# Kernel tuning notes

Hardware: AMD Instinct MI355X
Metric: run time of the kernel (lower is better)

Reference implementation:

```python
import jax, jax.numpy as jnp
import numpy as np
from jax import lax

B, T, DIN, E, F, U, H1, DOUT = 128, 1000, 64, 256, 64, 2, 80, 64
CLIP = 5.0
LVMIN = float(np.log(1e-4))


def _gru(wih, whh, bih, bhh, x, h):
    # PyTorch GRUCell math: gates ordered [r, z, n]
    gi = x @ wih.T + bih
    gh = h @ whh.T + bhh
    ir, iz, inn = jnp.split(gi, 3, axis=-1)
    hr, hz, hn = jnp.split(gh, 3, axis=-1)
    r = jax.nn.sigmoid(ir + hr)
    z = jax.nn.sigmoid(iz + hz)
    n = jnp.tanh(inn + r * hn)
    return (1.0 - z) * n + z * h


def setup_inputs() -> dict:
    key = jax.random.key(0)
    ks = iter(jax.random.split(key, 64))
    def nrm(shape, std=None):
        s = std if std is not None else shape[-1] ** -0.5
        return (jax.random.normal(next(ks), shape) * s).astype(jnp.float32)
    d = {}
    d['x'] = nrm((B, T, DIN), 1.0)
    d['eps_g0'] = nrm((B, E), 1.0)
    d['eps_u'] = nrm((B, T, U), 1.0)
    def gru_p(name, din):
        d[name + '_wih'] = nrm((3 * E, din))
        d[name + '_whh'] = nrm((3 * E, E))
        d[name + '_bih'] = jnp.zeros((3 * E,), jnp.float32)
        d[name + '_bhh'] = jnp.zeros((3 * E,), jnp.float32)
    gru_p('egf', DIN); gru_p('egb', DIN)          # g0 fwd/bwd encoders
    gru_p('ecf', DIN); gru_p('ecb', DIN)          # controller fwd/bwd encoders
    gru_p('con', 2 * E + F)                        # controller GRU
    gru_p('gen', U)                                # generator GRU
    def lin(name, dout, din):
        d[name + '_w'] = nrm((dout, din))
        d[name + '_b'] = jnp.zeros((dout,), jnp.float32)
    lin('g0m', E, 2 * E); lin('g0v', E, 2 * E)
    lin('um', U, E); lin('uv', U, E)
    lin('fac', F, E); lin('f1', H1, F); lin('cl', DOUT, H1)
    return d


def reference(x, eps_g0, eps_u,
              egf_wih, egf_whh, egf_bih, egf_bhh,
              egb_wih, egb_whh, egb_bih, egb_bhh,
              ecf_wih, ecf_whh, ecf_bih, ecf_bhh,
              ecb_wih, ecb_whh, ecb_bih, ecb_bhh,
              con_wih, con_whh, con_bih, con_bhh,
              gen_wih, gen_whh, gen_bih, gen_bhh,
              g0m_w, g0m_b, g0v_w, g0v_b,
              um_w, um_b, uv_w, uv_b,
              fac_w, fac_b, f1_w, f1_b, cl_w, cl_b):
    b = x.shape[0]
    xt = jnp.swapaxes(x, 0, 1)  # (T, B, DIN)
    h0 = jnp.zeros((b, E), x.dtype)

    # forward encoder pass: efgen (final only) + efcon (all states, clamped max)
    def fwd_step(carry, xt_):
        hg, hc = carry
        hg = jnp.minimum(_gru(egf_wih, egf_whh, egf_bih, egf_bhh, xt_, hg), CLIP)
        hc = jnp.minimum(_gru(ecf_wih, ecf_whh, ecf_bih, ecf_bhh, xt_, hc), CLIP)
        return (hg, hc), hc
    (hg_f, _), ef_states = lax.scan(fwd_step, (h0, h0), xt)  # ef_states[t] == efcon[:, t+1]

    def bwd_step(carry, xt_):
        hg, hc = carry
        hg = jnp.minimum(_gru(egb_wih, egb_whh, egb_bih, egb_bhh, xt_, hg), CLIP)
        hc = jnp.minimum(_gru(ecb_wih, ecb_whh, ecb_bih, ecb_bhh, xt_, hc), CLIP)
        return (hg, hc), hc
    (hg_b, _), eb_rev = lax.scan(bwd_step, (h0, h0), xt[::-1])
    eb_states = eb_rev[::-1]  # eb_states[t] == ebcon[:, t]

    # g0 posterior + sample + initial factors
    egen = jnp.concatenate([hg_f, hg_b], axis=-1)  # (B, 2E)
    g0_mean = egen @ g0m_w.T + g0m_b
    g0_logvar = jnp.maximum(egen @ g0v_w.T + g0v_b, LVMIN)
    g = eps_g0 * jnp.exp(0.5 * g0_logvar) + g0_mean
    f = g @ fac_w.T + fac_b

    # controller + generator scan
    def gen_step(carry, inp):
        c, g, f = carry
        ef_t, eb_t, eps = inp
        cin = jnp.concatenate([ef_t, eb_t, f], axis=-1)
        c = jnp.minimum(_gru(con_wih, con_whh, con_bih, con_bhh, cin, c), CLIP)
        u_mean = c @ um_w.T + um_b
        u_logvar = jnp.maximum(c @ uv_w.T + uv_b, LVMIN)
        u = eps * jnp.exp(0.5 * u_logvar) + u_mean
        g = jnp.minimum(_gru(gen_wih, gen_whh, gen_bih, gen_bhh, u, g), CLIP)
        f = g @ fac_w.T + fac_b
        out = jax.nn.relu(f @ f1_w.T + f1_b) @ cl_w.T + cl_b
        return (c, g, f), out

    eps_t = jnp.swapaxes(eps_u, 0, 1)  # (T, B, U)
    _, outs = lax.scan(gen_step, (h0, g, f), (ef_states, eb_states, eps_t))
    return jnp.swapaxes(outs, 0, 1)  # (B, T, DOUT)
```

## Files before the change

kernel.cpp:

```cpp
#include <hip/hip_runtime.h>
#include <stdint.h>
#include <stddef.h>


#define B_    128
#define T_    1000
#define DIN_  64
#define E_    256
#define F_    64
#define H1_   80
#define DOUT_ 64
#define CLIPV 5.0f
#define LVMIN_ (-9.210340371976182f)
#define TC_   128
#define NCHUNK_ 8

typedef _Float16 f16;
typedef _Float16 f16x2 __attribute__((ext_vector_type(2)));

__device__ __forceinline__ float sigm_(float x) { return 1.0f/(1.0f + expf(-x)); }

__device__ __forceinline__ float dot2_(f16x2 a, f16x2 b, float c) {
  asm("v_dot2_f32_f16 %0, %1, %2, %0" : "+v"(c) : "v"(a), "v"(b));
  return c;
}
#define P0_(Wv) __builtin_bit_cast(f16x2, (Wv).x)
#define P1_(Wv) __builtin_bit_cast(f16x2, (Wv).y)
#define P2_(Wv) __builtin_bit_cast(f16x2, (Wv).z)
#define P3_(Wv) __builtin_bit_cast(f16x2, (Wv).w)
#define DOT4(Av, Wv, Hv) \
  Av = dot2_(P0_(Wv), P0_(Hv), Av); Av = dot2_(P1_(Wv), P1_(Hv), Av); \
  Av = dot2_(P2_(Wv), P2_(Hv), Av); Av = dot2_(P3_(Wv), P3_(Hv), Av);


struct PEncArgs { const float* wih[4]; const float* whh[4]; f16* dst; };

__global__ __launch_bounds__(256) void k_prep_enc(PEncArgs a) {
  const int chain = blockIdx.y;
  const int idx = blockIdx.x*256 + threadIdx.x;
  float v;
  if (idx < 49152) {
    const int i = idx & 7, j = (idx >> 3) & 255;
    const int r = idx >> 11;
    const int m = r % 3, k8 = r / 3;
    v = a.wih[chain][((size_t)(m*E_ + j))*DIN_ + k8*8 + i];
  } else {
    const int t = idx - 49152;
    const int i = t & 7, j = (t >> 3) & 255;
    const int r = t >> 11;
    const int m = r % 3, k8 = r / 3;
    v = a.whh[chain][((size_t)(m*E_ + j))*E_ + k8*8 + i];
  }
  a.dst[(size_t)chain*245760 + idx] = (f16)v;
}

__global__ __launch_bounds__(256) void k_prep_gen(const float* __restrict__ conwhh,
                                                  const float* __restrict__ genwhh,
                                                  f16* __restrict__ wg6) {
  const int idx = blockIdx.x*256 + threadIdx.x;
  const int i = idx & 7, j = (idx >> 3) & 255;
  const int r = idx >> 11;
  const int m = r % 6, k8 = r / 6;
  const int k = k8*8 + i;
  const float v = (m < 3) ? conwhh[(size_t)(m*E_ + j)*E_ + k]
                          : genwhh[(size_t)((m-3)*E_ + j)*E_ + k];
  wg6[idx] = (f16)v;
}

__global__ __launch_bounds__(256) void k_prep_w3(const float* __restrict__ conwih,
                                                 f16* __restrict__ w3) {
  const int idx = blockIdx.x*256 + threadIdx.x;
  const int i = idx & 7, j = (idx >> 3) & 255;
  const int r = idx >> 11;
  const int m = r % 3, k8 = r / 3;
  w3[idx] = (f16)conwih[(size_t)(m*E_ + j)*576 + 512 + k8*8 + i];
}

__global__ __launch_bounds__(256) void k_prep_w2(const float* __restrict__ conwih,
                                                 f16* __restrict__ w2) {
  const int idx = blockIdx.x*256 + threadIdx.x;
  const int i = idx & 7, j = (idx >> 3) & 255;
  const int r = idx >> 11;
  const int m = r % 3, k8 = r / 3;
  w2[idx] = (f16)conwih[(size_t)(m*E_ + j)*576 + k8*8 + i];
}

__global__ void k_prep_bias(const float* __restrict__ conbih,
                            const float* __restrict__ conbhh,
                            const float* __restrict__ genbih,
                            const float* __restrict__ genbhh,
                            float* __restrict__ bias8) {
  const int j = threadIdx.x;
  float* o = bias8 + j*8;
  o[0] = conbih[j]      + conbhh[j];
  o[1] = conbih[E_+j]   + conbhh[E_+j];
  o[2] = conbih[2*E_+j];
  o[3] = conbhh[2*E_+j];
  o[4] = genbih[j]      + genbhh[j];
  o[5] = genbih[E_+j]   + genbhh[E_+j];
  o[6] = genbih[2*E_+j];
  o[7] = genbhh[2*E_+j];
}


struct EncArgs {
  const float* x;
  const float* bih[4]; const float* bhh[4];
  const f16* wenc;
  f16* efS; f16* ebS;
  float* hgF; float* hgB;
};

__global__ __launch_bounds__(1024) void k_encoder(EncArgs a) {
  __shared__ __align__(16) f16 shh[2][256];
  __shared__ __align__(16) f16 sxh[2][64];
  __shared__ float shf[2][256];
  __shared__ float sred[3][6][256];
  const int chain = blockIdx.x >> 6;
  const int pair  = blockIdx.x & 63;
  const int b0 = pair*2;
  const int j  = threadIdx.x & 255;
  const int kq = threadIdx.x >> 8;
  const bool bwd = (chain >= 2);
  const f16* Wih = a.wenc + (size_t)chain*245760;
  const f16* Whh = Wih + 49152;
  f16* st = (chain==1) ? a.efS : (chain==3 ? a.ebS : nullptr);
  float* hgout = (chain==0) ? a.hgF : (chain==2 ? a.hgB : nullptr);

  float br=0,bz=0,bni=0,bnh=0;
  if (kq == 0) {
    br  = a.bih[chain][j]      + a.bhh[chain][j];
    bz  = a.bih[chain][E_+j]   + a.bhh[chain][E_+j];
    bni = a.bih[chain][2*E_+j];
    bnh = a.bhh[chain][2*E_+j];
  }
  if (threadIdx.x < 512) {
    shf[threadIdx.x>>8][threadIdx.x&255] = 0.f;
    shh[threadIdx.x>>8][threadIdx.x&255] = (f16)0.f;
  }
  float xv = 0.f;
  if (kq == 0 && j < 128) {
    const int q = j >> 6, k = j & 63;
    const int tt0 = bwd ? (T_-1) : 0;
    xv = a.x[((size_t)(b0+q)*T_ + tt0)*DIN_ + k];
  }
  const f16* wpi = Wih + (size_t)j*8;
  const f16* wph = Whh + (size_t)j*8;

  for (int t = 0; t < T_; ++t) {
    const int tt = bwd ? (T_-1-t) : t;
    if (kq == 0 && j < 128) sxh[j>>6][j&63] = (f16)xv;
    __syncthreads();
    if (kq == 0 && j < 128 && t+1 < T_) {
      const int q = j >> 6, k = j & 63;
      const int tn = bwd ? (T_-2-t) : (t+1);
      xv = a.x[((size_t)(b0+q)*T_ + tn)*DIN_ + k];
    }
    float ar[2]={0,0}, az[2]={0,0}, ani[2]={0,0}, anh[2]={0,0};
    if (kq == 0) {
      #pragma unroll 2
      for (int k8 = 0; k8 < 8; ++k8) {
        const uint4 c0 = *(const uint4*)(wpi + (size_t)(k8*3+0)*2048);
        const uint4 c1 = *(const uint4*)(wpi + (size_t)(k8*3+1)*2048);
        const uint4 c2 = *(const uint4*)(wpi + (size_t)(k8*3+2)*2048);
        #pragma unroll
        for (int q = 0; q < 2; ++q) {
          const uint4 xq = *(const uint4*)(&sxh[q][k8*8]);
          DOT4(ar[q], c0, xq); DOT4(az[q], c1, xq); DOT4(ani[q], c2, xq);
        }
      }
      #pragma unroll
      for (int k8 = 0; k8 < 2; ++k8) {
        const uint4 c0 = *(const uint4*)(wph + (size_t)(k8*3+0)*2048);
        const uint4 c1 = *(const uint4*)(wph + (size_t)(k8*3+1)*2048);
        const uint4 c2 = *(const uint4*)(wph + (size_t)(k8*3+2)*2048);
        #pragma unroll
        for (int q = 0; q < 2; ++q) {
          const uint4 hq = *(const uint4*)(&shh[q][k8*8]);
          DOT4(ar[q], c0, hq); DOT4(az[q], c1, hq); DOT4(anh[q], c2, hq);
        }
      }
    } else {
      const int ks = 2 + (kq-1)*10;
      #pragma unroll 2
      for (int kk = 0; kk < 10; ++kk) {
        const int k8 = ks + kk;
        const uint4 c0 = *(const uint4*)(wph + (size_t)(k8*3+0)*2048);
        const uint4 c1 = *(const uint4*)(wph + (size_t)(k8*3+1)*2048);
        const uint4 c2 = *(const uint4*)(wph + (size_t)(k8*3+2)*2048);
        #pragma unroll
        for (int q = 0; q < 2; ++q) {
          const uint4 hq = *(const uint4*)(&shh[q][k8*8]);
          DOT4(ar[q], c0, hq); DOT4(az[q], c1, hq); DOT4(anh[q], c2, hq);
        }
      }
      #pragma unroll
      for (int q = 0; q < 2; ++q) {
        sred[kq-1][q*3+0][j] = ar[q];
        sred[kq-1][q*3+1][j] = az[q];
        sred[kq-1][q*3+2][j] = anh[q];
      }
    }
    __syncthreads();
    if (kq == 0) {
      #pragma unroll
      for (int q = 0; q < 2; ++q) {
        const float arq  = ar[q]  + sred[0][q*3+0][j] + sred[1][q*3+0][j]
                         + sred[2][q*3+0][j] + br;
        const float azq  = az[q]  + sred[0][q*3+1][j] + sred[1][q*3+1][j]
                         + sred[2][q*3+1][j] + bz;
        const float anhq = anh[q] + sred[0][q*3+2][j] + sred[1][q*3+2][j]
                         + sred[2][q*3+2][j] + bnh;
        const float r = sigm_(arq);
        const float z = sigm_(azq);
        const float n = tanhf(ani[q] + bni + r*anhq);
        const float hn = fminf((1.f - z)*n + z*shf[q][j], CLIPV);
        shf[q][j] = hn;
        shh[q][j] = (f16)hn;
        if (st) st[((size_t)(b0+q)*T_ + tt)*E_ + j] = (f16)hn;
        if (hgout && t == T_-1) hgout[(size_t)(b0+q)*E_ + j] = hn;
      }
    }
  }
}


__global__ __launch_bounds__(256) void k_g0(const float* __restrict__ hgF,
                                            const float* __restrict__ hgB,
                                            const float* __restrict__ g0mw,
                                            const float* __restrict__ g0mb,
                                            const float* __restrict__ g0vw,
                                            const float* __restrict__ g0vb,
                                            const float* __restrict__ epsg0,
                                            float* __restrict__ S) {
  __shared__ __align__(16) float sf[E_], sb[E_];
  const int b = blockIdx.x, k = threadIdx.x;
  sf[k] = hgF[(size_t)b*E_ + k];
  sb[k] = hgB[(size_t)b*E_ + k];
  __syncthreads();
  const float* mr = g0mw + (size_t)k*512;
  const float* vr = g0vw + (size_t)k*512;
  float dm = 0.f, dv = 0.f;
  for (int i = 0; i < E_; i += 4) {
    const float4 m4 = *(const float4*)(mr + i);
    const float4 v4 = *(const float4*)(vr + i);
    const float4 h4 = *(const float4*)&sf[i];
    dm += m4.x*h4.x + m4.y*h4.y + m4.z*h4.z + m4.w*h4.w;
    dv += v4.x*h4.x + v4.y*h4.y + v4.z*h4.z + v4.w*h4.w;
  }
  for (int i = 0; i < E_; i += 4) {
    const float4 m4 = *(const float4*)(mr + 256 + i);
    const float4 v4 = *(const float4*)(vr + 256 + i);
    const float4 h4 = *(const float4*)&sb[i];
    dm += m4.x*h4.x + m4.y*h4.y + m4.z*h4.z + m4.w*h4.w;
    dv += v4.x*h4.x + v4.y*h4.y + v4.z*h4.z + v4.w*h4.w;
  }
  const float lv = fmaxf(dv + g0vb[k], LVMIN_);
  const float g  = epsg0[(size_t)b*E_ + k]*expf(0.5f*lv) + dm + g0mb[k];
  S[(size_t)b*512 + k]       = g;
  S[(size_t)b*512 + 256 + k] = 0.f;
}


struct GeArgs { const f16* efS; const f16* ebS; const f16* w2; f16* ge; int t0; };

__global__ __launch_bounds__(256) void k_ge(GeArgs a) {
  __shared__ __align__(16) f16 A[8][512];
  const int tile = blockIdx.x, b = blockIdx.y;
  const int tl0 = tile*8;
  const int j = threadIdx.x;
  for (int r = 0; r < 16; ++r) {
    const int idx = r*256 + j;
    const int tt = idx >> 9, k = idx & 511;
    const int t = a.t0 + tl0 + tt;
    f16 v = (f16)0.f;
    if (t < T_)
      v = (k < 256) ? a.efS[((size_t)b*T_ + t)*E_ + k]
                    : a.ebS[((size_t)b*T_ + t)*E_ + (k-256)];
    A[tt][k] = v;
  }
  __syncthreads();
  float acc[3][8];
  #pragma unroll
  for (int m = 0; m < 3; ++m)
    #pragma unroll
    for (int tt = 0; tt < 8; ++tt) acc[m][tt] = 0.f;
  const f16* wb = a.w2 + (size_t)j*8;
  #pragma unroll 2
  for (int k8 = 0; k8 < 64; ++k8) {
    uint4 av[8];
    #pragma unroll
    for (int tt = 0; tt < 8; ++tt) av[tt] = *(const uint4*)&A[tt][k8*8];
    #pragma unroll
    for (int m = 0; m < 3; ++m) {
      const uint4 wm = *(const uint4*)(wb + (size_t)(k8*3+m)*2048);
      DOT4(acc[m][0], wm, av[0]); DOT4(acc[m][1], wm, av[1]);
      DOT4(acc[m][2], wm, av[2]); DOT4(acc[m][3], wm, av[3]);
      DOT4(acc[m][4], wm, av[4]); DOT4(acc[m][5], wm, av[5]);
      DOT4(acc[m][6], wm, av[6]); DOT4(acc[m][7], wm, av[7]);
    }
  }
  #pragma unroll
  for (int m = 0; m < 3; ++m)
    #pragma unroll
    for (int tt = 0; tt < 8; ++tt)
      a.ge[((size_t)b*TC_ + tl0+tt)*768 + m*E_ + j] = (f16)acc[m][tt];
}


struct GenArgs {
  const f16* wg6;
  const f16* w3;
  const f16* ge;
  const float* bias8;
  const float* genwih;
  const float* umw; const float* umb; const float* uvw; const float* uvb;
  const float* epsu;
  const float* facw; const float* facb;
  float* S;
  char* fout;
  int t0, tcnt;
};

__global__ __launch_bounds__(1024) void k_gen(GenArgs a) {
  __shared__ __align__(16) f16 sgh[256], sch[256], sfh[64];
  __shared__ float sgf[256], scf[256];
  __shared__ float sred[3][7][256];
  __shared__ float s_ured[4][4];
  __shared__ __align__(16) f16 sfac2[16384];
  __shared__ float s_fred[16][64];
  const int b = blockIdx.x;
  const int tid = threadIdx.x;
  const int j  = tid & 255;
  const int kq = tid >> 8;
  const int lane = tid & 63;
  const int wv = (tid >> 6) & 3;

  for (int idx = tid; idx < 16384; idx += 1024) {
    const int k = idx >> 6, d = idx & 63;
    sfac2[(size_t)(k>>1)*128 + d*2 + (k&1)] = (f16)a.facw[(size_t)d*E_ + k];
  }
  if (kq == 0) {
    const float g0v = a.S[(size_t)b*512 + j];
    const float c0v = a.S[(size_t)b*512 + 256 + j];
    sgf[j] = g0v; sgh[j] = (f16)g0v;
    scf[j] = c0v; sch[j] = (f16)c0v;
  }
  float b_rc=0,b_zc=0,b_nc=0,b_nhc=0,b_rg=0,b_zg=0,b_ng=0,b_nhg=0;
  float gur0=0,gur1=0,guz0=0,guz1=0,gun0=0,gun1=0;
  float uwm0=0,uwm1=0,uwv0=0,uwv1=0,umb0=0,umb1=0,uvb0=0,uvb1=0;
  float facb_l = 0.f;
  if (kq == 0) {
    const float* B8 = a.bias8 + j*8;
    b_rc=B8[0]; b_zc=B8[1]; b_nc=B8[2]; b_nhc=B8[3];
    b_rg=B8[4]; b_zg=B8[5]; b_ng=B8[6]; b_nhg=B8[7];
    gur0 = a.genwih[j*2];          gur1 = a.genwih[j*2+1];
    guz0 = a.genwih[(E_+j)*2];     guz1 = a.genwih[(E_+j)*2+1];
    gun0 = a.genwih[(2*E_+j)*2];   gun1 = a.genwih[(2*E_+j)*2+1];
    uwm0 = a.umw[j]; uwm1 = a.umw[E_+j];
    uwv0 = a.uvw[j]; uwv1 = a.uvw[E_+j];
    umb0 = a.umb[0]; umb1 = a.umb[1];
    uvb0 = a.uvb[0]; uvb1 = a.uvb[1];
  }
  if (tid < 64) facb_l = a.facb[tid];
  const f16* wb6 = a.wg6 + (size_t)j*8;
  const f16* wb3 = a.w3  + (size_t)j*8;
  __syncthreads();

  {
    const int d = tid & 63, grp = tid >> 6;
    float fp = 0.f;
    #pragma unroll
    for (int k2 = grp*8; k2 < grp*8+8; ++k2)
      fp = dot2_(*(const f16x2*)(sfac2 + (size_t)(k2*64 + d)*2),
                 *(const f16x2*)(&sgh[k2*2]), fp);
    s_fred[grp][d] = fp;
  }
  __syncthreads();
  if (tid < 64) {
    float fv = facb_l;
    #pragma unroll
    for (int g = 0; g < 16; ++g) fv += s_fred[g][tid];
    sfh[tid] = (f16)fv;
  }
  __syncthreads();

  for (int tl = 0; tl < a.tcnt; ++tl) {
    const int t = a.t0 + tl;
    float ge_r=0, ge_z=0, ge_n=0;
    float2 ev = {0,0};
    if (kq == 0) {
      const f16* gp = a.ge + ((size_t)b*TC_ + tl)*768;
      ge_r = (float)gp[j]; ge_z = (float)gp[E_+j]; ge_n = (float)gp[2*E_+j];
      ev = *(const float2*)(a.epsu + ((size_t)b*T_ + t)*2);
    }
    float ar=0, az=0, ani=0, anh=0, gr=0, gz=0, gh=0;
    {
      const int ks = kq*9;
      const int ke = (kq==3) ? 32 : ks+9;
      #pragma unroll 2
      for (int k8 = ks; k8 < ke; ++k8) {
        const f16* wk = wb6 + (size_t)k8*6*2048;
        const uint4 gv = *(const uint4*)&sgh[k8*8];
        const uint4 cv = *(const uint4*)&sch[k8*8];
        uint4 ww;
        ww = *(const uint4*)(wk + 0*2048); DOT4(ar, ww, cv);
        ww = *(const uint4*)(wk + 1*2048); DOT4(az, ww, cv);
        ww = *(const uint4*)(wk + 2*2048); DOT4(anh, ww, cv);
        ww = *(const uint4*)(wk + 3*2048); DOT4(gr, ww, gv);
        ww = *(const uint4*)(wk + 4*2048); DOT4(gz, ww, gv);
        ww = *(const uint4*)(wk + 5*2048); DOT4(gh, ww, gv);
      }
      if (kq == 3) {
        #pragma unroll 2
        for (int k8 = 0; k8 < 8; ++k8) {
          const f16* wk = wb3 + (size_t)k8*3*2048;
          const uint4 fv4 = *(const uint4*)&sfh[k8*8];
          uint4 ww;
          ww = *(const uint4*)(wk + 0*2048); DOT4(ar, ww, fv4);
          ww = *(const uint4*)(wk + 1*2048); DOT4(az, ww, fv4);
          ww = *(const uint4*)(wk + 2*2048); DOT4(ani, ww, fv4);
        }
      }
    }
    if (kq) {
      sred[kq-1][0][j]=ar; sred[kq-1][1][j]=az; sred[kq-1][2][j]=ani;
      sred[kq-1][3][j]=anh; sred[kq-1][4][j]=gr; sred[kq-1][5][j]=gz;
      sred[kq-1][6][j]=gh;
    }
    __syncthreads();
    float grt=0, gzt=0, ght=0;
    if (kq == 0) {
      const float art  = ar + sred[0][0][j]+sred[1][0][j]+sred[2][0][j]
                       + ge_r + b_rc;
      const float azt  = az + sred[0][1][j]+sred[1][1][j]+sred[2][1][j]
                       + ge_z + b_zc;
      const float anit = ani + sred[0][2][j]+sred[1][2][j]+sred[2][2][j]
                       + ge_n + b_nc;
      const float anht = anh + sred[0][3][j]+sred[1][3][j]+sred[2][3][j]
                       + b_nhc;
      grt = gr + sred[0][4][j]+sred[1][4][j]+sred[2][4][j];
      gzt = gz + sred[0][5][j]+sred[1][5][j]+sred[2][5][j];
      ght = gh + sred[0][6][j]+sred[1][6][j]+sred[2][6][j];
      const float r = sigm_(art), z = sigm_(azt);
      const float n = tanhf(anit + r*anht);
      const float cn = fminf((1.f-z)*n + z*scf[j], CLIPV);
      scf[j] = cn; sch[j] = (f16)cn;
      float p0=uwm0*cn, p1=uwm1*cn, p2=uwv0*cn, p3=uwv1*cn;
      #pragma unroll
      for (int s = 32; s; s >>= 1) {
        p0+=__shfl_down(p0,s); p1+=__shfl_down(p1,s);
        p2+=__shfl_down(p2,s); p3+=__shfl_down(p3,s);
      }
      if (lane == 0) {
        s_ured[wv][0]=p0; s_ured[wv][1]=p1; s_ured[wv][2]=p2; s_ured[wv][3]=p3;
      }
    }
    __syncthreads();
    if (kq == 0) {
      const float sm0 = s_ured[0][0]+s_ured[1][0]+s_ured[2][0]+s_ured[3][0];
      const float sm1 = s_ured[0][1]+s_ured[1][1]+s_ured[2][1]+s_ured[3][1];
      const float sm2 = s_ured[0][2]+s_ured[1][2]+s_ured[2][2]+s_ured[3][2];
      const float sm3 = s_ured[0][3]+s_ured[1][3]+s_ured[2][3]+s_ured[3][3];
      const float lv0 = fmaxf(sm2 + uvb0, LVMIN_);
      const float lv1 = fmaxf(sm3 + uvb1, LVMIN_);
      const float u0 = ev.x*expf(0.5f*lv0) + sm0 + umb0;
      const float u1 = ev.y*expf(0.5f*lv1) + sm1 + umb1;
      const float rg = sigm_(grt + gur0*u0 + gur1*u1 + b_rg);
      const float zg = sigm_(gzt + guz0*u0 + guz1*u1 + b_zg);
      const float ng = tanhf(gun0*u0 + gun1*u1 + b_ng + rg*(ght + b_nhg));
      const float gn = fminf((1.f-zg)*ng + zg*sgf[j], CLIPV);
      sgf[j] = gn; sgh[j] = (f16)gn;
    }
    __syncthreads();
    {
      const int d = tid & 63, grp = tid >> 6;
      float fp = 0.f;
      #pragma unroll
      for (int k2 = grp*8; k2 < grp*8+8; ++k2)
        fp = dot2_(*(const f16x2*)(sfac2 + (size_t)(k2*64 + d)*2),
                   *(const f16x2*)(&sgh[k2*2]), fp);
      s_fred[grp][d] = fp;
    }
    __syncthreads();
    if (tid < 64) {
      float fv = facb_l;
      #pragma unroll
      for (int g = 0; g < 16; ++g) fv += s_fred[g][tid];
      float* fo = (float*)(a.fout + ((size_t)b*T_ + t)*512);
      fo[tid] = fv;
      sfh[tid] = (f16)fv;
    }
    __syncthreads();
  }
  if (kq == 0) {
    a.S[(size_t)b*512 + j]       = sgf[j];
    a.S[(size_t)b*512 + 256 + j] = scf[j];
  }
}


struct MlpArgs { const char* fbase; const float* f1w; const float* f1b;
                 const float* clw; const float* clb; float* out; };

__global__ __launch_bounds__(256) void k_mlp(MlpArgs a) {
  __shared__ float sf1T[64*80];
  __shared__ float sclT[80*64];
  __shared__ float sfv[4][64];
  __shared__ float sh1[4][80];
  const int b = blockIdx.y, t0 = blockIdx.x*8;
  const int j = threadIdx.x, lane = j & 63, w = j >> 6;
  for (int idx = j; idx < 5120; idx += 256) {
    const int k = idx / 80, d = idx % 80;
    sf1T[idx] = a.f1w[(size_t)d*64 + k];
  }
  for (int idx = j; idx < 5120; idx += 256) {
    const int kh = idx >> 6, o = idx & 63;
    sclT[idx] = a.clw[(size_t)o*80 + kh];
  }
  __syncthreads();
  for (int ti = 0; ti < 2; ++ti) {
    const int t = t0 + w*2 + ti;
    const float* fp = (const float*)(a.fbase + ((size_t)b*T_ + t)*512);
    sfv[w][lane] = fp[lane];
    __syncthreads();
    float h1a = a.f1b[lane];
    float h1b = (lane < 16) ? a.f1b[64 + lane] : 0.f;
    for (int k = 0; k < 64; ++k) {
      const float fv = sfv[w][k];
      h1a += sf1T[k*80 + lane]*fv;
      if (lane < 16) h1b += sf1T[k*80 + 64 + lane]*fv;
    }
    sh1[w][lane] = fmaxf(h1a, 0.f);
    if (lane < 16) sh1[w][64 + lane] = fmaxf(h1b, 0.f);
    __syncthreads();
    float o = a.clb[lane];
    for (int kh = 0; kh < H1_; ++kh)
      o += sclT[kh*64 + lane]*sh1[w][kh];
    a.out[((size_t)b*T_ + t)*DOUT_ + lane] = o;
    __syncthreads();
  }
}


extern "C" void kernel_launch(void* const* d_in, const int* in_sizes, int n_in,
                              void* d_out, int out_size, void* d_ws, size_t ws_size,
                              hipStream_t stream) {
  const float* x      = (const float*)d_in[0];
  const float* eps_g0 = (const float*)d_in[1];
  const float* eps_u  = (const float*)d_in[2];
  const float* egf_wih = (const float*)d_in[3],  *egf_whh = (const float*)d_in[4];
  const float* egf_bih = (const float*)d_in[5],  *egf_bhh = (const float*)d_in[6];
  const float* egb_wih = (const float*)d_in[7],  *egb_whh = (const float*)d_in[8];
  const float* egb_bih = (const float*)d_in[9],  *egb_bhh = (const float*)d_in[10];
  const float* ecf_wih = (const float*)d_in[11], *ecf_whh = (const float*)d_in[12];
  const float* ecf_bih = (const float*)d_in[13], *ecf_bhh = (const float*)d_in[14];
  const float* ecb_wih = (const float*)d_in[15], *ecb_whh = (const float*)d_in[16];
  const float* ecb_bih = (const float*)d_in[17], *ecb_bhh = (const float*)d_in[18];
  const float* con_wih = (const float*)d_in[19], *con_whh = (const float*)d_in[20];
  const float* con_bih = (const float*)d_in[21], *con_bhh = (const float*)d_in[22];
  const float* gen_wih = (const float*)d_in[23], *gen_whh = (const float*)d_in[24];
  const float* gen_bih = (const float*)d_in[25], *gen_bhh = (const float*)d_in[26];
  const float* g0m_w = (const float*)d_in[27], *g0m_b = (const float*)d_in[28];
  const float* g0v_w = (const float*)d_in[29], *g0v_b = (const float*)d_in[30];
  const float* um_w = (const float*)d_in[31], *um_b = (const float*)d_in[32];
  const float* uv_w = (const float*)d_in[33], *uv_b = (const float*)d_in[34];
  const float* fac_w = (const float*)d_in[35], *fac_b = (const float*)d_in[36];
  const float* f1_w = (const float*)d_in[37], *f1_b = (const float*)d_in[38];
  const float* cl_w = (const float*)d_in[39], *cl_b = (const float*)d_in[40];
  float* out = (float*)d_out;
  (void)ws_size; (void)in_sizes; (void)n_in; (void)out_size;

  char* ws = (char*)d_ws;
  f16* efS   = (f16*)(ws + 0);
  f16* ebS   = (f16*)(ws + 65536000ul);
  f16* geb   = (f16*)(ws + 131072000ul);
  f16* wenc  = (f16*)(ws + 156237824ul);
  f16* wg6   = (f16*)(ws + 158203904ul);
  f16* w3    = (f16*)(ws + 158990336ul);
  f16* w2    = (f16*)(ws + 159088640ul);
  float* hgF = (float*)(ws + 159875072ul);
  float* hgB = (float*)(ws + 160006144ul);
  float* S   = (float*)(ws + 160137216ul);
  float* bias8 = (float*)(ws + 160399360ul);

  PEncArgs pe;
  pe.wih[0] = egf_wih; pe.whh[0] = egf_whh;
  pe.wih[1] = ecf_wih; pe.whh[1] = ecf_whh;
  pe.wih[2] = egb_wih; pe.whh[2] = egb_whh;
  pe.wih[3] = ecb_wih; pe.whh[3] = ecb_whh;
  pe.dst = wenc;
  k_prep_enc<<<dim3(960, 4), 256, 0, stream>>>(pe);
  k_prep_gen<<<1536, 256, 0, stream>>>(con_whh, gen_whh, wg6);
  k_prep_w3<<<192, 256, 0, stream>>>(con_wih, w3);
  k_prep_w2<<<1536, 256, 0, stream>>>(con_wih, w2);
  k_prep_bias<<<1, 256, 0, stream>>>(con_bih, con_bhh, gen_bih, gen_bhh, bias8);

  EncArgs ea;
  ea.x = x;
  ea.bih[0] = egf_bih; ea.bhh[0] = egf_bhh;
  ea.bih[1] = ecf_bih; ea.bhh[1] = ecf_bhh;
  ea.bih[2] = egb_bih; ea.bhh[2] = egb_bhh;
  ea.bih[3] = ecb_bih; ea.bhh[3] = ecb_bhh;
  ea.wenc = wenc; ea.efS = efS; ea.ebS = ebS; ea.hgF = hgF; ea.hgB = hgB;
  k_encoder<<<256, 1024, 0, stream>>>(ea);

  k_g0<<<128, 256, 0, stream>>>(hgF, hgB, g0m_w, g0m_b, g0v_w, g0v_b, eps_g0, S);

  for (int c = 0; c < NCHUNK_; ++c) {
    GeArgs ga; ga.efS = efS; ga.ebS = ebS; ga.w2 = w2; ga.ge = geb; ga.t0 = c*TC_;
    k_ge<<<dim3(16, B_), 256, 0, stream>>>(ga);
    GenArgs gn;
    gn.wg6 = wg6; gn.w3 = w3; gn.ge = geb; gn.bias8 = bias8; gn.genwih = gen_wih;
    gn.umw = um_w; gn.umb = um_b; gn.uvw = uv_w; gn.uvb = uv_b;
    gn.epsu = eps_u; gn.facw = fac_w; gn.facb = fac_b;
    gn.S = S; gn.fout = (char*)ws;
    gn.t0 = c*TC_;
    gn.tcnt = (T_ - c*TC_ < TC_) ? (T_ - c*TC_) : TC_;
    k_gen<<<128, 1024, 0, stream>>>(gn);
  }

  MlpArgs ma; ma.fbase = (const char*)ws; ma.f1w = f1_w; ma.f1b = f1_b;
  ma.clw = cl_w; ma.clb = cl_b; ma.out = out;
  k_mlp<<<dim3(125, B_), 256, 0, stream>>>(ma);
}
```

Before: 14.77 ms.

## Overlap next-chunk input projection with generator scan and cache weights in registers

Result: no change. 15.00 ms (+1.5%).

```diff
diff --git a/kernel.cpp b/kernel.cpp
--- a/kernel.cpp
+++ b/kernel.cpp
@@ -12,8 +12,8 @@
 #define DOUT_ 64
 #define CLIPV 5.0f
 #define LVMIN_ (-9.210340371976182f)
-#define TC_   128
-#define NCHUNK_ 8
+#define TC_   64
+#define NCHUNK_ 16
 
 typedef _Float16 f16;
 typedef _Float16 f16x2 __attribute__((ext_vector_type(2)));
@@ -146,6 +146,18 @@
   }
   const f16* wpi = Wih + (size_t)j*8;
   const f16* wph = Whh + (size_t)j*8;
+  const int ks1 = 2 + (kq-1)*10;
+
+  uint4 RC[12];
+  if (kq == 0) {
+    #pragma unroll
+    for (int i = 0; i < 12; ++i)
+      RC[i] = *(const uint4*)(wpi + (size_t)i*2048);
+  } else {
+    #pragma unroll
+    for (int i = 0; i < 12; ++i)
+      RC[i] = *(const uint4*)(wph + (size_t)(ks1*3 + i)*2048);
+  }
 
   for (int t = 0; t < T_; ++t) {
     const int tt = bwd ? (T_-1-t) : t;
@@ -158,8 +170,17 @@
     }
     float ar[2]={0,0}, az[2]={0,0}, ani[2]={0,0}, anh[2]={0,0};
     if (kq == 0) {
+      #pragma unroll
+      for (int k8 = 0; k8 < 4; ++k8) {
+        #pragma unroll
+        for (int q = 0; q < 2; ++q) {
+          const uint4 xq = *(const uint4*)(&sxh[q][k8*8]);
+          DOT4(ar[q], RC[k8*3+0], xq); DOT4(az[q], RC[k8*3+1], xq);
+          DOT4(ani[q], RC[k8*3+2], xq);
+        }
+      }
       #pragma unroll 2
-      for (int k8 = 0; k8 < 8; ++k8) {
+      for (int k8 = 4; k8 < 8; ++k8) {
         const uint4 c0 = *(const uint4*)(wpi + (size_t)(k8*3+0)*2048);
         const uint4 c1 = *(const uint4*)(wpi + (size_t)(k8*3+1)*2048);
         const uint4 c2 = *(const uint4*)(wpi + (size_t)(k8*3+2)*2048);
@@ -181,10 +202,19 @@
         }
       }
     } else {
-      const int ks = 2 + (kq-1)*10;
+      #pragma unroll
+      for (int i = 0; i < 4; ++i) {
+        const int k8 = ks1 + i;
+        #pragma unroll
+        for (int q = 0; q < 2; ++q) {
+          const uint4 hq = *(const uint4*)(&shh[q][k8*8]);
+          DOT4(ar[q], RC[i*3+0], hq); DOT4(az[q], RC[i*3+1], hq);
+          DOT4(anh[q], RC[i*3+2], hq);
+        }
+      }
       #pragma unroll 2
-      for (int kk = 0; kk < 10; ++kk) {
-        const int k8 = ks + kk;
+      for (int kk = 4; kk < 10; ++kk) {
+        const int k8 = ks1 + kk;
         const uint4 c0 = *(const uint4*)(wph + (size_t)(k8*3+0)*2048);
         const uint4 c1 = *(const uint4*)(wph + (size_t)(k8*3+1)*2048);
         const uint4 c2 = *(const uint4*)(wph + (size_t)(k8*3+2)*2048);
@@ -319,18 +349,70 @@
   const float* facw; const float* facb;
   float* S;
   char* fout;
-  int t0, tcnt;
+  const f16* efS; const f16* ebS; const f16* w2;
+  f16* genext;
+  int t0, tcnt, t0n;
 };
 
-__global__ __launch_bounds__(1024) void k_gen(GenArgs a) {
+__global__ __launch_bounds__(1024) void k_genge(GenArgs a) {
   __shared__ __align__(16) f16 sgh[256], sch[256], sfh[64];
   __shared__ float sgf[256], scf[256];
   __shared__ float sred[3][7][256];
   __shared__ float s_ured[4][4];
   __shared__ __align__(16) f16 sfac2[16384];
   __shared__ float s_fred[16][64];
+  __shared__ __align__(16) f16 Age[4][8][512];
+  const int tid = threadIdx.x;
+
+  if (blockIdx.x >= 128) {
+    if (a.t0n >= T_) return;
+    const int bb = blockIdx.x - 128;
+    const int grp = tid >> 8, jt = tid & 255;
+    f16* A = &Age[grp][0][0];
+    const f16* wb = a.w2 + (size_t)jt*8;
+    for (int ti = 0; ti < 2; ++ti) {
+      const int tl0 = (grp*2 + ti)*8;
+      for (int r = 0; r < 16; ++r) {
+        const int idx = r*256 + jt;
+        const int tt = idx >> 9, k = idx & 511;
+        const int t = a.t0n + tl0 + tt;
+        f16 v = (f16)0.f;
+        if (t < T_)
+          v = (k < 256) ? a.efS[((size_t)bb*T_ + t)*E_ + k]
+                        : a.ebS[((size_t)bb*T_ + t)*E_ + (k-256)];
+        A[tt*512 + k] = v;
+      }
+      __syncthreads();
+      float acc[3][8];
+      #pragma unroll
+      for (int m = 0; m < 3; ++m)
+        #pragma unroll
+        for (int tt = 0; tt < 8; ++tt) acc[m][tt] = 0.f;
+      #pragma unroll 2
+      for (int k8 = 0; k8 < 64; ++k8) {
+        uint4 av[8];
+        #pragma unroll
+        for (int tt = 0; tt < 8; ++tt) av[tt] = *(const uint4*)&A[tt*512 + k8*8];
+        #pragma unroll
+        for (int m = 0; m < 3; ++m) {
+          const uint4 wm = *(const uint4*)(wb + (size_t)(k8*3+m)*2048);
+          DOT4(acc[m][0], wm, av[0]); DOT4(acc[m][1], wm, av[1]);
+          DOT4(acc[m][2], wm, av[2]); DOT4(acc[m][3], wm, av[3]);
+          DOT4(acc[m][4], wm, av[4]); DOT4(acc[m][5], wm, av[5]);
+          DOT4(acc[m][6], wm, av[6]); DOT4(acc[m][7], wm, av[7]);
+        }
+      }
+      #pragma unroll
+      for (int m = 0; m < 3; ++m)
+        #pragma unroll
+        for (int tt = 0; tt < 8; ++tt)
+          a.genext[((size_t)bb*TC_ + tl0+tt)*768 + m*E_ + jt] = (f16)acc[m][tt];
+      __syncthreads();
+    }
+    return;
+  }
+
   const int b = blockIdx.x;
-  const int tid = threadIdx.x;
   const int j  = tid & 255;
   const int kq = tid >> 8;
   const int lane = tid & 63;
@@ -365,6 +447,15 @@
   if (tid < 64) facb_l = a.facb[tid];
   const f16* wb6 = a.wg6 + (size_t)j*8;
   const f16* wb3 = a.w3  + (size_t)j*8;
+  const int ks = kq*9;
+  const int ke = (kq==3) ? 32 : ks+9;
+
+  uint4 GC[12];
+  #pragma unroll
+  for (int i = 0; i < 2; ++i)
+    #pragma unroll
+    for (int m = 0; m < 6; ++m)
+      GC[i*6+m] = *(const uint4*)(wb6 + ((size_t)(ks+i)*6 + m)*2048);
   __syncthreads();
 
   {
@@ -396,10 +487,20 @@
     }
     float ar=0, az=0, ani=0, anh=0, gr=0, gz=0, gh=0;
     {
-      const int ks = kq*9;
-      const int ke = (kq==3) ? 32 : ks+9;
+      #pragma unroll
+      for (int i = 0; i < 2; ++i) {
+        const int k8 = ks + i;
+        const uint4 gv = *(const uint4*)&sgh[k8*8];
+        const uint4 cv = *(const uint4*)&sch[k8*8];
+        DOT4(ar,  GC[i*6+0], cv);
+        DOT4(az,  GC[i*6+1], cv);
+        DOT4(anh, GC[i*6+2], cv);
+        DOT4(gr,  GC[i*6+3], gv);
+        DOT4(gz,  GC[i*6+4], gv);
+        DOT4(gh,  GC[i*6+5], gv);
+      }
       #pragma unroll 2
-      for (int k8 = ks; k8 < ke; ++k8) {
+      for (int k8 = ks+2; k8 < ke; ++k8) {
         const f16* wk = wb6 + (size_t)k8*6*2048;
         const uint4 gv = *(const uint4*)&sgh[k8*8];
         const uint4 cv = *(const uint4*)&sch[k8*8];
@@ -574,7 +675,8 @@
   char* ws = (char*)d_ws;
   f16* efS   = (f16*)(ws + 0);
   f16* ebS   = (f16*)(ws + 65536000ul);
-  f16* geb   = (f16*)(ws + 131072000ul);
+  f16* geb0  = (f16*)(ws + 131072000ul);
+  f16* geb1  = (f16*)(ws + 131072000ul + 12582912ul);
   f16* wenc  = (f16*)(ws + 156237824ul);
   f16* wg6   = (f16*)(ws + 158203904ul);
   f16* w3    = (f16*)(ws + 158990336ul);
@@ -607,17 +709,25 @@
 
   k_g0<<<128, 256, 0, stream>>>(hgF, hgB, g0m_w, g0m_b, g0v_w, g0v_b, eps_g0, S);
 
+  {
+    GeArgs ga; ga.efS = efS; ga.ebS = ebS; ga.w2 = w2; ga.ge = geb0; ga.t0 = 0;
+    k_ge<<<dim3(8, B_), 256, 0, stream>>>(ga);
+  }
+
   for (int c = 0; c < NCHUNK_; ++c) {
-    GeArgs ga; ga.efS = efS; ga.ebS = ebS; ga.w2 = w2; ga.ge = geb; ga.t0 = c*TC_;
-    k_ge<<<dim3(16, B_), 256, 0, stream>>>(ga);
     GenArgs gn;
-    gn.wg6 = wg6; gn.w3 = w3; gn.ge = geb; gn.bias8 = bias8; gn.genwih = gen_wih;
+    gn.wg6 = wg6; gn.w3 = w3;
+    gn.ge = (c & 1) ? geb1 : geb0;
+    gn.bias8 = bias8; gn.genwih = gen_wih;
     gn.umw = um_w; gn.umb = um_b; gn.uvw = uv_w; gn.uvb = uv_b;
     gn.epsu = eps_u; gn.facw = fac_w; gn.facb = fac_b;
     gn.S = S; gn.fout = (char*)ws;
+    gn.efS = efS; gn.ebS = ebS; gn.w2 = w2;
+    gn.genext = ((c+1) & 1) ? geb1 : geb0;
     gn.t0 = c*TC_;
     gn.tcnt = (T_ - c*TC_ < TC_) ? (T_ - c*TC_) : TC_;
-    k_gen<<<128, 1024, 0, stream>>>(gn);
+    gn.t0n = (c+1)*TC_;
+    k_genge<<<256, 1024, 0, stream>>>(gn);
   }
 
   MlpArgs ma; ma.fbase = (const char*)ws; ma.f1w = f1_w; ma.f1b = f1_b;
```
